# Kernel optimization log

Measured on AMD Instinct MI355X. Metric: run time of the kernel, lower is better.

The kernel has to match this reference:

```python
import jax, jax.numpy as jnp
import numpy as np

H, FFN, NH = 1024, 4096, 16
DK = H // NH
SCALE = DK ** -0.5


def _ln(x, g, b, eps=1e-5):
    m = jnp.mean(x, axis=-1, keepdims=True)
    v = jnp.var(x, axis=-1, keepdims=True)
    return (x - m) * jax.lax.rsqrt(v + eps) * g + b


def setup_inputs() -> dict:
    key = jax.random.key(0)
    ks = jax.random.split(key, 16)
    B, S = 4, 2048
    s = lambda fan: fan ** -0.5
    d = {
        "x": jax.random.normal(ks[0], (B, S, H), jnp.float32),
        "attn_bias": jax.random.normal(ks[1], (1, NH, S, S), jnp.float32),
        "ln1_g": jnp.ones((H,), jnp.float32),
        "ln1_b": jnp.zeros((H,), jnp.float32),
        "Wq": jax.random.normal(ks[2], (H, H), jnp.float32) * s(H),
        "bq": jnp.zeros((H,), jnp.float32),
        "Wk": jax.random.normal(ks[3], (H, H), jnp.float32) * s(H),
        "bk": jnp.zeros((H,), jnp.float32),
        "Wv": jax.random.normal(ks[4], (H, H), jnp.float32) * s(H),
        "bv": jnp.zeros((H,), jnp.float32),
        "Wo": jax.random.normal(ks[5], (H, H), jnp.float32) * s(H),
        "bo": jnp.zeros((H,), jnp.float32),
        "ln2_g": jnp.ones((H,), jnp.float32),
        "ln2_b": jnp.zeros((H,), jnp.float32),
        "W1": jax.random.normal(ks[6], (H, FFN), jnp.float32) * s(H),
        "b1": jnp.zeros((FFN,), jnp.float32),
        "W2": jax.random.normal(ks[7], (FFN, H), jnp.float32) * s(FFN),
        "b2": jnp.zeros((H,), jnp.float32),
    }
    return d


def reference(x, attn_bias, ln1_g, ln1_b, Wq, bq, Wk, bk, Wv, bv, Wo, bo,
              ln2_g, ln2_b, W1, b1, W2, b2):
    B, S, _ = x.shape
    y = _ln(x, ln1_g, ln1_b)
    q = (y @ Wq + bq).reshape(B, S, NH, DK)
    k = (y @ Wk + bk).reshape(B, S, NH, DK)
    v = (y @ Wv + bv).reshape(B, S, NH, DK)
    scores = jnp.einsum("bqhd,bkhd->bhqk", q * SCALE, k) + attn_bias
    A = jax.nn.softmax(scores, axis=-1)
    out = jnp.einsum("bhqk,bkhd->bqhd", A, v).reshape(B, S, H)
    x = x + (out @ Wo + bo)
    y = _ln(x, ln2_g, ln2_b)
    y = jax.nn.gelu(y @ W1 + b1, approximate=False) @ W2 + b2
    return x + y
```

## Files before the change

kernel.cpp:

```cpp
#include <hip/hip_runtime.h>

#define DEVINL __device__ __forceinline__

typedef __bf16 bf16x8 __attribute__((ext_vector_type(8)));
typedef float f32x4 __attribute__((ext_vector_type(4)));
typedef unsigned short u16x4 __attribute__((ext_vector_type(4)));

static constexpr int Bb = 4, S = 2048, H = 1024, NH = 16, DK = 64, FF = 4096;
static constexpr int Mrows = Bb * S;
static constexpr int QS = 3 * H;

DEVINL unsigned short f2bf(float f) {
    union { __bf16 b; unsigned short u; } r;
    r.b = (__bf16)f;
    return r.u;
}

DEVINL unsigned pack_bf2(float a, float b) {
    union { __bf16 h[2]; unsigned u; } r;
    r.h[0] = (__bf16)a; r.h[1] = (__bf16)b;
    return r.u;
}

DEVINL void gld16(const void* g, void* l) {
    auto gp = reinterpret_cast<const __attribute__((address_space(1))) unsigned*>(
        reinterpret_cast<unsigned long long>(g));
    auto lp = reinterpret_cast<__attribute__((address_space(3))) unsigned*>(
        (unsigned)reinterpret_cast<unsigned long long>(l));
    __builtin_amdgcn_global_load_lds(gp, lp, 16, 0, 0);
}

__global__ __launch_bounds__(256)
void wcvt_all(const float* __restrict__ Wq, const float* __restrict__ Wk,
              const float* __restrict__ Wv, const float* __restrict__ Wo,
              const float* __restrict__ W1, const float* __restrict__ W2,
              const float* __restrict__ bq, const float* __restrict__ bk2,
              const float* __restrict__ bv2,
              unsigned short* __restrict__ Wqt, unsigned short* __restrict__ Wot,
              unsigned short* __restrict__ W1t, unsigned short* __restrict__ W2t,
              float* __restrict__ bqkv) {
    int id = blockIdx.x;
    if (id >= 12288) {
        int i = (id - 12288) * 256 + threadIdx.y * 32 + threadIdx.x;
        float v = (i < 1024) ? bq[i] : (i < 2048 ? bk2[i - 1024] : bv2[i - 2048]);
        bqkv[i] = v;
        return;
    }
    const float* in; unsigned short* out; int K, N;
    if (id < 3072) {
        int which = id >> 10; id &= 1023;
        in = which == 0 ? Wq : (which == 1 ? Wk : Wv);
        out = Wqt + (size_t)which * H * H; K = H; N = H;
    } else if (id < 4096) { in = Wo; out = Wot; K = H; N = H; id -= 3072; }
    else if (id < 8192)   { in = W1; out = W1t; K = H; N = FF; id -= 4096; }
    else                  { in = W2; out = W2t; K = FF; N = H; id -= 8192; }
    const int nx = N / 32;
    const int n0 = (id % nx) * 32, k0 = (id / nx) * 32;

    __shared__ float t[32][33];
    int tx = threadIdx.x, ty = threadIdx.y;
#pragma unroll
    for (int i = 0; i < 32; i += 8) t[ty + i][tx] = in[(size_t)(k0 + ty + i) * N + n0 + tx];
    __syncthreads();
#pragma unroll
    for (int i = 0; i < 32; i += 8) out[(size_t)(n0 + ty + i) * K + k0 + tx] = f2bf(t[tx][ty + i]);
}

__global__ __launch_bounds__(256)
void ln_kernel(const float* __restrict__ x, const float* __restrict__ g,
               const float* __restrict__ be, unsigned short* __restrict__ y) {
    int row = blockIdx.x, tid = threadIdx.x;
    const float4 v = ((const float4*)(x + (size_t)row * H))[tid];
    float s = v.x + v.y + v.z + v.w;
    float ss = v.x * v.x + v.y * v.y + v.z * v.z + v.w * v.w;
#pragma unroll
    for (int m = 1; m < 64; m <<= 1) { s += __shfl_xor(s, m); ss += __shfl_xor(ss, m); }
    __shared__ float red[2][4];
    int lane = tid & 63, w = tid >> 6;
    if (lane == 0) { red[0][w] = s; red[1][w] = ss; }
    __syncthreads();
    s = red[0][0] + red[0][1] + red[0][2] + red[0][3];
    ss = red[1][0] + red[1][1] + red[1][2] + red[1][3];
    float mean = s * (1.f / H);
    float var = ss * (1.f / H) - mean * mean;
    float rstd = rsqrtf(var + 1e-5f);
    float4 gv = ((const float4*)g)[tid];
    float4 bv = ((const float4*)be)[tid];
    ushort4 o;
    o.x = f2bf((v.x - mean) * rstd * gv.x + bv.x);
    o.y = f2bf((v.y - mean) * rstd * gv.y + bv.y);
    o.z = f2bf((v.z - mean) * rstd * gv.z + bv.z);
    o.w = f2bf((v.w - mean) * rstd * gv.w + bv.w);
    ((ushort4*)(y + (size_t)row * H))[tid] = o;
}

template <int EPI>
__global__ __launch_bounds__(512, 2)
void gemm8p(const unsigned short* __restrict__ A, const unsigned short* __restrict__ Bt,
            const float* __restrict__ bias, void* __restrict__ outp, int N, int K) {
    __shared__ __align__(16) char lds[131072];
    const int tid = threadIdx.x, lane = tid & 63, w = tid >> 6;
    const int wm = w >> 2, wn = w & 3;
    const int fr = lane & 15, fq = lane >> 4;
    const int nwg = gridDim.x, id = blockIdx.x;
    const int swz = (id & 7) * (nwg >> 3) + (id >> 3);
    const int m0 = (swz & 31) * 256, n0 = (swz >> 5) * 256;

    int srow[2], scol[2];
#pragma unroll
    for (int l = 0; l < 2; ++l) {
        int idx = l * 512 + tid;
        srow[l] = idx >> 3;
        scol[l] = ((idx & 7) ^ (srow[l] & 7)) * 8;
    }
    const int NT = K >> 6;

    auto stage = [&](int ht, int buf, int kt) {
        const unsigned short* src = (ht < 2) ? A : Bt;
        const int hh = ht & 1;
        char* dst = lds + ((ht < 2 ? 0 : 65536) + (buf * 2 + hh) * 16384);
        const int rbase = ((ht < 2) ? m0 : n0) + hh * 128;
        const int kb = kt * 64;
#pragma unroll
        for (int l = 0; l < 2; ++l)
            gld16(src + (size_t)(rbase + srow[l]) * K + kb + scol[l],
                  dst + (size_t)(l * 512 + tid) * 16);
    };

    int oa[2];
#pragma unroll
    for (int ks = 0; ks < 2; ++ks)
        oa[ks] = fr * 128 + (((ks * 4 + fq) ^ (fr & 7)) & 7) * 16;
    const int aBase0 = wm * 16384;
    const int bBase0 = 65536 + (wn >> 1) * 16384 + (wn & 1) * 8192;

    f32x4 acc[8][4] = {};
    bf16x8 aF[4][2], bF[4][2];

    stage(0, 0, 0); stage(1, 0, 0); stage(2, 0, 0); stage(3, 0, 0);
    if (NT > 1) {
        stage(0, 1, 1);
        asm volatile("s_waitcnt vmcnt(2)" ::: "memory");
    } else {
        asm volatile("s_waitcnt vmcnt(0)" ::: "memory");
    }
    __builtin_amdgcn_s_barrier();

    int buf = 0;
    for (int t = 0; t < NT; ++t, buf ^= 1) {
        const char* Ar = lds + aBase0 + buf * 32768;
        const char* Br = lds + bBase0 + buf * 32768;

#pragma unroll
        for (int mb = 0; mb < 4; ++mb)
#pragma unroll
            for (int ks = 0; ks < 2; ++ks)
                aF[mb][ks] = *(const bf16x8*)(Ar + mb * 2048 + oa[ks]);
#pragma unroll
        for (int nb = 0; nb < 2; ++nb)
#pragma unroll
            for (int ks = 0; ks < 2; ++ks)
                bF[nb][ks] = *(const bf16x8*)(Br + nb * 2048 + oa[ks]);
        if (t + 1 < NT) stage(1, buf ^ 1, t + 1);
        __builtin_amdgcn_s_barrier();
        asm volatile("s_waitcnt lgkmcnt(0)" ::: "memory");
        __builtin_amdgcn_sched_barrier(0);
        __builtin_amdgcn_s_setprio(1);
#pragma unroll
        for (int mb = 0; mb < 4; ++mb)
#pragma unroll
            for (int nb = 0; nb < 2; ++nb)
#pragma unroll
                for (int ks = 0; ks < 2; ++ks)
                    acc[mb][nb] = __builtin_amdgcn_mfma_f32_16x16x32_bf16(aF[mb][ks], bF[nb][ks], acc[mb][nb], 0, 0, 0);
        __builtin_amdgcn_s_setprio(0);
        __builtin_amdgcn_s_barrier();

#pragma unroll
        for (int nb = 2; nb < 4; ++nb)
#pragma unroll
            for (int ks = 0; ks < 2; ++ks)
                bF[nb][ks] = *(const bf16x8*)(Br + nb * 2048 + oa[ks]);
        if (t + 1 < NT) stage(2, buf ^ 1, t + 1);
        __builtin_amdgcn_s_barrier();
        asm volatile("s_waitcnt lgkmcnt(0)" ::: "memory");
        __builtin_amdgcn_sched_barrier(0);
        __builtin_amdgcn_s_setprio(1);
#pragma unroll
        for (int mb = 0; mb < 4; ++mb)
#pragma unroll
            for (int nb = 2; nb < 4; ++nb)
#pragma unroll
                for (int ks = 0; ks < 2; ++ks)
                    acc[mb][nb] = __builtin_amdgcn_mfma_f32_16x16x32_bf16(aF[mb][ks], bF[nb][ks], acc[mb][nb], 0, 0, 0);
        __builtin_amdgcn_s_setprio(0);
        __builtin_amdgcn_s_barrier();

#pragma unroll
        for (int mb = 0; mb < 4; ++mb)
#pragma unroll
            for (int ks = 0; ks < 2; ++ks)
                aF[mb][ks] = *(const bf16x8*)(Ar + 8192 + mb * 2048 + oa[ks]);
        if (t + 1 < NT) stage(3, buf ^ 1, t + 1);
        __builtin_amdgcn_s_barrier();
        asm volatile("s_waitcnt lgkmcnt(0)" ::: "memory");
        __builtin_amdgcn_sched_barrier(0);
        __builtin_amdgcn_s_setprio(1);
#pragma unroll
        for (int mb = 0; mb < 4; ++mb)
#pragma unroll
            for (int nb = 0; nb < 2; ++nb)
#pragma unroll
                for (int ks = 0; ks < 2; ++ks)
                    acc[4 + mb][nb] = __builtin_amdgcn_mfma_f32_16x16x32_bf16(aF[mb][ks], bF[nb][ks], acc[4 + mb][nb], 0, 0, 0);
        __builtin_amdgcn_s_setprio(0);
        __builtin_amdgcn_s_barrier();

        if (t + 2 < NT) {
            stage(0, buf, t + 2);
            asm volatile("s_waitcnt vmcnt(2)" ::: "memory");
        } else if (t + 1 < NT) {
            asm volatile("s_waitcnt vmcnt(0)" ::: "memory");
        }
        __builtin_amdgcn_s_barrier();
        __builtin_amdgcn_s_setprio(1);
#pragma unroll
        for (int mb = 0; mb < 4; ++mb)
#pragma unroll
            for (int nb = 2; nb < 4; ++nb)
#pragma unroll
                for (int ks = 0; ks < 2; ++ks)
                    acc[4 + mb][nb] = __builtin_amdgcn_mfma_f32_16x16x32_bf16(aF[mb][ks], bF[nb][ks], acc[4 + mb][nb], 0, 0, 0);
        __builtin_amdgcn_s_setprio(0);
        __builtin_amdgcn_s_barrier();
    }

#pragma unroll
    for (int mb = 0; mb < 8; ++mb) {
        int row0 = m0 + wm * 128 + mb * 16 + fq * 4;
#pragma unroll
        for (int nb = 0; nb < 4; ++nb) {
            int col = n0 + wn * 64 + nb * 16 + fr;
            float bz = bias[col];
#pragma unroll
            for (int j = 0; j < 4; ++j) {
                float vv = acc[mb][nb][j] + bz;
                size_t idx = (size_t)(row0 + j) * N + col;
                if (EPI == 0) {
                    ((unsigned short*)outp)[idx] = f2bf(vv);
                } else {
                    float tg = 0.5f * vv * (1.f + erff(vv * 0.70710678118654752f));
                    ((unsigned short*)outp)[idx] = f2bf(tg);
                }
            }
        }
    }
}

template <int EPI>
__global__ __launch_bounds__(512, 2)
void gemm8p128(const unsigned short* __restrict__ A, const unsigned short* __restrict__ Bt,
               const float* __restrict__ bias, const float* __restrict__ resid,
               void* __restrict__ outp, int N, int K) {
    __shared__ __align__(16) char lds[98304];
    const int tid = threadIdx.x, lane = tid & 63, w = tid >> 6;
    const int wm = w >> 2, wn = w & 3;
    const int fr = lane & 15, fq = lane >> 4;
    const int nwg = gridDim.x, id = blockIdx.x;
    const int swz = (id & 7) * (nwg >> 3) + (id >> 3);
    const int m0 = (swz & 63) * 128, n0 = (swz >> 6) * 256;

    int srow[2], scol[2];
#pragma unroll
    for (int l = 0; l < 2; ++l) {
        int idx = l * 512 + tid;
        srow[l] = idx >> 3;
        scol[l] = ((idx & 7) ^ (srow[l] & 7)) * 8;
    }
    const int NT = K >> 6;

    auto stageA = [&](int buf, int kt) {
        char* dst = lds + buf * 16384;
#pragma unroll
        for (int l = 0; l < 2; ++l)
            gld16(A + (size_t)(m0 + srow[l]) * K + kt * 64 + scol[l],
                  dst + (size_t)(l * 512 + tid) * 16);
    };
    auto stageB = [&](int hh, int buf, int kt) {
        char* dst = lds + 32768 + buf * 32768 + hh * 16384;
#pragma unroll
        for (int l = 0; l < 2; ++l)
            gld16(Bt + (size_t)(n0 + hh * 128 + srow[l]) * K + kt * 64 + scol[l],
                  dst + (size_t)(l * 512 + tid) * 16);
    };

    int oa[2];
#pragma unroll
    for (int ks = 0; ks < 2; ++ks)
        oa[ks] = fr * 128 + (((ks * 4 + fq) ^ (fr & 7)) & 7) * 16;
    const int aWB = wm * 8192;
    const int bWB = (wn >> 1) * 16384 + (wn & 1) * 8192;

    f32x4 acc[4][4] = {};
    bf16x8 aF[2][2], bF[4][2];

    stageA(0, 0); stageB(0, 0, 0); stageB(1, 0, 0);
    if (NT > 1) {
        stageA(1, 1);
        asm volatile("s_waitcnt vmcnt(2)" ::: "memory");
    } else {
        asm volatile("s_waitcnt vmcnt(0)" ::: "memory");
    }
    __builtin_amdgcn_s_barrier();

    int buf = 0;
    for (int t = 0; t < NT; ++t, buf ^= 1) {
        const char* Ar = lds + buf * 16384 + aWB;
        const char* Br = lds + 32768 + buf * 32768 + bWB;

#pragma unroll
        for (int mb = 0; mb < 2; ++mb)
#pragma unroll
            for (int ks = 0; ks < 2; ++ks)
                aF[mb][ks] = *(const bf16x8*)(Ar + mb * 2048 + oa[ks]);
#pragma unroll
        for (int nb = 0; nb < 2; ++nb)
#pragma unroll
            for (int ks = 0; ks < 2; ++ks)
                bF[nb][ks] = *(const bf16x8*)(Br + nb * 2048 + oa[ks]);
        if (t + 1 < NT) stageB(0, buf ^ 1, t + 1);
        __builtin_amdgcn_s_barrier();
        asm volatile("s_waitcnt lgkmcnt(0)" ::: "memory");
        __builtin_amdgcn_sched_barrier(0);
        __builtin_amdgcn_s_setprio(1);
#pragma unroll
        for (int mb = 0; mb < 2; ++mb)
#pragma unroll
            for (int nb = 0; nb < 2; ++nb)
#pragma unroll
                for (int ks = 0; ks < 2; ++ks)
                    acc[mb][nb] = __builtin_amdgcn_mfma_f32_16x16x32_bf16(aF[mb][ks], bF[nb][ks], acc[mb][nb], 0, 0, 0);
        __builtin_amdgcn_s_setprio(0);
        __builtin_amdgcn_s_barrier();

#pragma unroll
        for (int nb = 2; nb < 4; ++nb)
#pragma unroll
            for (int ks = 0; ks < 2; ++ks)
                bF[nb][ks] = *(const bf16x8*)(Br + nb * 2048 + oa[ks]);
        if (t + 1 < NT) stageB(1, buf ^ 1, t + 1);
        __builtin_amdgcn_s_barrier();
        asm volatile("s_waitcnt lgkmcnt(0)" ::: "memory");
        __builtin_amdgcn_sched_barrier(0);
        __builtin_amdgcn_s_setprio(1);
#pragma unroll
        for (int mb = 0; mb < 2; ++mb)
#pragma unroll
            for (int nb = 2; nb < 4; ++nb)
#pragma unroll
                for (int ks = 0; ks < 2; ++ks)
                    acc[mb][nb] = __builtin_amdgcn_mfma_f32_16x16x32_bf16(aF[mb][ks], bF[nb][ks], acc[mb][nb], 0, 0, 0);
        __builtin_amdgcn_s_setprio(0);
        __builtin_amdgcn_s_barrier();

#pragma unroll
        for (int mb = 0; mb < 2; ++mb)
#pragma unroll
            for (int ks = 0; ks < 2; ++ks)
                aF[mb][ks] = *(const bf16x8*)(Ar + 4096 + mb * 2048 + oa[ks]);
        __builtin_amdgcn_s_barrier();
        asm volatile("s_waitcnt lgkmcnt(0)" ::: "memory");
        __builtin_amdgcn_sched_barrier(0);
        __builtin_amdgcn_s_setprio(1);
#pragma unroll
        for (int mb = 0; mb < 2; ++mb)
#pragma unroll
            for (int nb = 0; nb < 2; ++nb)
#pragma unroll
                for (int ks = 0; ks < 2; ++ks)
                    acc[2 + mb][nb] = __builtin_amdgcn_mfma_f32_16x16x32_bf16(aF[mb][ks], bF[nb][ks], acc[2 + mb][nb], 0, 0, 0);
        __builtin_amdgcn_s_setprio(0);
        __builtin_amdgcn_s_barrier();

        if (t + 2 < NT) {
            stageA(buf, t + 2);
            asm volatile("s_waitcnt vmcnt(2)" ::: "memory");
        } else if (t + 1 < NT) {
            asm volatile("s_waitcnt vmcnt(0)" ::: "memory");
        }
        __builtin_amdgcn_s_barrier();
        __builtin_amdgcn_s_setprio(1);
#pragma unroll
        for (int mb = 0; mb < 2; ++mb)
#pragma unroll
            for (int nb = 2; nb < 4; ++nb)
#pragma unroll
                for (int ks = 0; ks < 2; ++ks)
                    acc[2 + mb][nb] = __builtin_amdgcn_mfma_f32_16x16x32_bf16(aF[mb][ks], bF[nb][ks], acc[2 + mb][nb], 0, 0, 0);
        __builtin_amdgcn_s_setprio(0);
        __builtin_amdgcn_s_barrier();
    }

#pragma unroll
    for (int mb = 0; mb < 4; ++mb) {
        int row0 = m0 + wm * 64 + mb * 16 + fq * 4;
#pragma unroll
        for (int nb = 0; nb < 4; ++nb) {
            int col = n0 + wn * 64 + nb * 16 + fr;
            float bz = bias[col];
#pragma unroll
            for (int j = 0; j < 4; ++j) {
                size_t idx = (size_t)(row0 + j) * N + col;
                float vv = acc[mb][nb][j] + bz;
                if (EPI == 0) {
                    ((unsigned short*)outp)[idx] = f2bf(vv);
                } else {
                    ((float*)outp)[idx] = vv + resid[idx];
                }
            }
        }
    }
}

__global__ __launch_bounds__(512, 4)
void attn_kernel(const unsigned short* __restrict__ QKV, const float* __restrict__ bias,
                 unsigned short* __restrict__ O) {
    __shared__ __align__(16) unsigned short lK[3][4096];
    __shared__ __align__(16) unsigned short lV[3][4096];
    const int tid = threadIdx.x, lane = tid & 63, w = tid >> 6;
    const int fr = lane & 15, fq = lane >> 4;

    const int bid = blockIdx.x;
    const int slice = (bid >> 5) * 8 + (bid & 7);
    const int b = (bid >> 3) & 3;
    const int h = slice >> 4;
    const int q0 = (slice & 15) * 128;

    const size_t base = (size_t)b * S * QS + h * DK;
    const unsigned short* Qp = QKV + base;
    const unsigned short* Kp = QKV + base + H;
    const unsigned short* Vp = QKV + base + 2 * H;
    const size_t obase = (size_t)b * S * H + h * DK;

    bf16x8 aq[2];
    {
        const unsigned short* qp = Qp + (size_t)(q0 + w * 16 + fr) * QS + fq * 8;
        aq[0] = *(const bf16x8*)qp;
        aq[1] = *(const bf16x8*)(qp + 32);
    }

    const int chk = w * 64 + lane;
    const int rK = chk >> 3, cK = ((chk & 7) ^ (rK & 7)) * 8;
    int vk, vd;
    {
        int ch = chk;
        int dch = ch & 1, j = (ch >> 1) & 3, fqi = (ch >> 3) & 3, half = (ch >> 5) & 1,
            c = (ch >> 6) & 3, ks = (ch >> 8) & 1;
        vk = ks * 32 + half * 16 + fqi * 4 + j; vd = c * 16 + dch * 8;
    }

    f32x4 oacc[4] = {};
    float lrun = 0.f;
    const float* bias_q = bias + (size_t)h * S * S + (size_t)(q0 + w * 16 + fr) * S;

    const float SC = 0.18033688f;
    const float BL = 1.44269504f;
    const float CC = -23.08312065f;

    auto stage = [&](int buf, int k0) {
        gld16(Kp + (size_t)(k0 + rK) * QS + cK, &lK[buf][w * 512]);
        gld16(Vp + (size_t)(k0 + vk) * QS + vd, &lV[buf][w * 512]);
    };

    union pa_t { unsigned u[4]; bf16x8 v; };
    pa_t pa0, pa1;

    stage(0, 0);
    __syncthreads();
    stage(1, 64);

    {
        float4 bv4[4];
#pragma unroll
        for (int c = 0; c < 4; ++c)
            bv4[c] = *(const float4*)(bias_q + c * 16 + fq * 4);
        f32x4 sacc[4] = {};
        __builtin_amdgcn_s_setprio(1);
#pragma unroll
        for (int c = 0; c < 4; ++c) {
            int row = c * 16 + fr;
#pragma unroll
            for (int dh = 0; dh < 2; ++dh) {
                bf16x8 bk = *(const bf16x8*)((char*)&lK[0][0] +
                    ((row * 128 + dh * 64 + fq * 16) ^ ((row & 7) << 4)));
                sacc[c] = __builtin_amdgcn_mfma_f32_16x16x32_bf16(bk, aq[dh], sacc[c], 0, 0, 0);
            }
        }
        __builtin_amdgcn_s_setprio(0);
        float p[4][4];
#pragma unroll
        for (int c = 0; c < 4; ++c) {
            float b0 = fmaf(bv4[c].x, BL, CC);
            float b1 = fmaf(bv4[c].y, BL, CC);
            float b2 = fmaf(bv4[c].z, BL, CC);
            float b3 = fmaf(bv4[c].w, BL, CC);
            p[c][0] = exp2f(fmaf(sacc[c][0], SC, b0));
            p[c][1] = exp2f(fmaf(sacc[c][1], SC, b1));
            p[c][2] = exp2f(fmaf(sacc[c][2], SC, b2));
            p[c][3] = exp2f(fmaf(sacc[c][3], SC, b3));
            lrun += p[c][0] + p[c][1] + p[c][2] + p[c][3];
        }
        pa0.u[0] = pack_bf2(p[0][0], p[0][1]);
        pa0.u[1] = pack_bf2(p[0][2], p[0][3]);
        pa0.u[2] = pack_bf2(p[1][0], p[1][1]);
        pa0.u[3] = pack_bf2(p[1][2], p[1][3]);
        pa1.u[0] = pack_bf2(p[2][0], p[2][1]);
        pa1.u[1] = pack_bf2(p[2][2], p[2][3]);
        pa1.u[2] = pack_bf2(p[3][0], p[3][1]);
        pa1.u[3] = pack_bf2(p[3][2], p[3][3]);
    }

    int bST = 2, bQK = 1, bPV = 0;
    for (int kt = 1; kt < S / 64; ++kt) {
        __syncthreads();
        if (kt + 1 < S / 64) stage(bST, (kt + 1) * 64);

        float4 bv4[4];
#pragma unroll
        for (int c = 0; c < 4; ++c)
            bv4[c] = *(const float4*)(bias_q + kt * 64 + c * 16 + fq * 4);

        u16x4 ra0[4], rb0[4], ra1[4], rb1[4];
        {
            const char* v0 = (const char*)&lV[bPV][0];
            const char* v1 = v0 + 4096;
#pragma unroll
            for (int c = 0; c < 4; ++c) {
                unsigned ad = (unsigned)(unsigned long long)(v0 + c * 1024) + lane * 8;
                asm volatile("ds_read_b64_tr_b16 %0, %1" : "=&v"(ra0[c]) : "v"(ad));
                asm volatile("ds_read_b64_tr_b16 %0, %1 offset:512" : "=&v"(rb0[c]) : "v"(ad));
            }
#pragma unroll
            for (int c = 0; c < 4; ++c) {
                unsigned ad = (unsigned)(unsigned long long)(v1 + c * 1024) + lane * 8;
                asm volatile("ds_read_b64_tr_b16 %0, %1" : "=&v"(ra1[c]) : "v"(ad));
                asm volatile("ds_read_b64_tr_b16 %0, %1 offset:512" : "=&v"(rb1[c]) : "v"(ad));
            }
        }
        __builtin_amdgcn_sched_barrier(0);

        f32x4 sacc[4] = {};
        __builtin_amdgcn_s_setprio(1);
#pragma unroll
        for (int c = 0; c < 4; ++c) {
            int row = c * 16 + fr;
#pragma unroll
            for (int dh = 0; dh < 2; ++dh) {
                bf16x8 bk = *(const bf16x8*)((char*)&lK[bQK][0] +
                    ((row * 128 + dh * 64 + fq * 16) ^ ((row & 7) << 4)));
                sacc[c] = __builtin_amdgcn_mfma_f32_16x16x32_bf16(bk, aq[dh], sacc[c], 0, 0, 0);
            }
        }
        __builtin_amdgcn_s_setprio(0);

        {
            asm volatile("s_waitcnt lgkmcnt(0)" ::: "memory");
            __builtin_amdgcn_sched_barrier(0);
            __builtin_amdgcn_s_setprio(1);
#pragma unroll
            for (int c = 0; c < 4; ++c) {
                union { u16x4 h2[2]; bf16x8 v8; } u;
                u.h2[0] = ra0[c]; u.h2[1] = rb0[c];
                oacc[c] = __builtin_amdgcn_mfma_f32_16x16x32_bf16(pa0.v, u.v8, oacc[c], 0, 0, 0);
            }
#pragma unroll
            for (int c = 0; c < 4; ++c) {
                union { u16x4 h2[2]; bf16x8 v8; } u;
                u.h2[0] = ra1[c]; u.h2[1] = rb1[c];
                oacc[c] = __builtin_amdgcn_mfma_f32_16x16x32_bf16(pa1.v, u.v8, oacc[c], 0, 0, 0);
            }
            __builtin_amdgcn_s_setprio(0);
            __builtin_amdgcn_sched_barrier(0);
        }

        {
            float p[4][4];
#pragma unroll
            for (int c = 0; c < 4; ++c) {
                float b0 = fmaf(bv4[c].x, BL, CC);
                float b1 = fmaf(bv4[c].y, BL, CC);
                float b2 = fmaf(bv4[c].z, BL, CC);
                float b3 = fmaf(bv4[c].w, BL, CC);
                p[c][0] = exp2f(fmaf(sacc[c][0], SC, b0));
                p[c][1] = exp2f(fmaf(sacc[c][1], SC, b1));
                p[c][2] = exp2f(fmaf(sacc[c][2], SC, b2));
                p[c][3] = exp2f(fmaf(sacc[c][3], SC, b3));
                lrun += p[c][0] + p[c][1] + p[c][2] + p[c][3];
            }
            pa0.u[0] = pack_bf2(p[0][0], p[0][1]);
            pa0.u[1] = pack_bf2(p[0][2], p[0][3]);
            pa0.u[2] = pack_bf2(p[1][0], p[1][1]);
            pa0.u[3] = pack_bf2(p[1][2], p[1][3]);
            pa1.u[0] = pack_bf2(p[2][0], p[2][1]);
            pa1.u[1] = pack_bf2(p[2][2], p[2][3]);
            pa1.u[2] = pack_bf2(p[3][0], p[3][1]);
            pa1.u[3] = pack_bf2(p[3][2], p[3][3]);
        }

        bPV = bQK; bQK = bST; bST = (bST == 2) ? 0 : bST + 1;
    }

    {
        const char* v0 = (const char*)&lV[bPV][0];
        const char* v1 = v0 + 4096;
        u16x4 ra0[4], rb0[4], ra1[4], rb1[4];
#pragma unroll
        for (int c = 0; c < 4; ++c) {
            unsigned ad = (unsigned)(unsigned long long)(v0 + c * 1024) + lane * 8;
            asm volatile("ds_read_b64_tr_b16 %0, %1" : "=&v"(ra0[c]) : "v"(ad));
            asm volatile("ds_read_b64_tr_b16 %0, %1 offset:512" : "=&v"(rb0[c]) : "v"(ad));
        }
#pragma unroll
        for (int c = 0; c < 4; ++c) {
            unsigned ad = (unsigned)(unsigned long long)(v1 + c * 1024) + lane * 8;
            asm volatile("ds_read_b64_tr_b16 %0, %1" : "=&v"(ra1[c]) : "v"(ad));
            asm volatile("ds_read_b64_tr_b16 %0, %1 offset:512" : "=&v"(rb1[c]) : "v"(ad));
        }
        asm volatile("s_waitcnt lgkmcnt(0)" ::: "memory");
        __builtin_amdgcn_sched_barrier(0);
        __builtin_amdgcn_s_setprio(1);
#pragma unroll
        for (int c = 0; c < 4; ++c) {
            union { u16x4 h2[2]; bf16x8 v8; } u;
            u.h2[0] = ra0[c]; u.h2[1] = rb0[c];
            oacc[c] = __builtin_amdgcn_mfma_f32_16x16x32_bf16(pa0.v, u.v8, oacc[c], 0, 0, 0);
        }
#pragma unroll
        for (int c = 0; c < 4; ++c) {
            union { u16x4 h2[2]; bf16x8 v8; } u;
            u.h2[0] = ra1[c]; u.h2[1] = rb1[c];
            oacc[c] = __builtin_amdgcn_mfma_f32_16x16x32_bf16(pa1.v, u.v8, oacc[c], 0, 0, 0);
        }
        __builtin_amdgcn_s_setprio(0);
    }

    lrun += __shfl_xor(lrun, 16);
    lrun += __shfl_xor(lrun, 32);
    float linv = 1.f / lrun;
    float lo[4];
#pragma unroll
    for (int j = 0; j < 4; ++j) lo[j] = __shfl(linv, fq * 4 + j);
#pragma unroll
    for (int c = 0; c < 4; ++c)
#pragma unroll
        for (int j = 0; j < 4; ++j) {
            int row = q0 + w * 16 + fq * 4 + j;
            int d = c * 16 + fr;
            O[obase + (size_t)row * H + d] = f2bf(oacc[c][j] * lo[j]);
        }
}

extern "C" void kernel_launch(void* const* d_in, const int* in_sizes, int n_in,
                              void* d_out, int out_size, void* d_ws, size_t ws_size,
                              hipStream_t stream) {
    const float* x    = (const float*)d_in[0];
    const float* ab   = (const float*)d_in[1];
    const float* ln1g = (const float*)d_in[2];
    const float* ln1b = (const float*)d_in[3];
    const float* Wq   = (const float*)d_in[4];
    const float* bq   = (const float*)d_in[5];
    const float* Wk   = (const float*)d_in[6];
    const float* bk   = (const float*)d_in[7];
    const float* Wv   = (const float*)d_in[8];
    const float* bv   = (const float*)d_in[9];
    const float* Wo   = (const float*)d_in[10];
    const float* bo   = (const float*)d_in[11];
    const float* ln2g = (const float*)d_in[12];
    const float* ln2b = (const float*)d_in[13];
    const float* W1   = (const float*)d_in[14];
    const float* b1   = (const float*)d_in[15];
    const float* W2   = (const float*)d_in[16];
    const float* b2   = (const float*)d_in[17];

    char* ws = (char*)d_ws;
    size_t off = 0;
    auto alloc = [&](size_t bytes) -> void* {
        void* p = ws + off;
        off += (bytes + 255) & ~(size_t)255;
        return p;
    };
    unsigned short* Wqt = (unsigned short*)alloc((size_t)H * H * 2);
    unsigned short* Wkt = (unsigned short*)alloc((size_t)H * H * 2);
    unsigned short* Wvt = (unsigned short*)alloc((size_t)H * H * 2);
    unsigned short* Wot = (unsigned short*)alloc((size_t)H * H * 2);
    unsigned short* W1t = (unsigned short*)alloc((size_t)H * FF * 2);
    unsigned short* W2t = (unsigned short*)alloc((size_t)H * FF * 2);
    float* bqkv        = (float*)alloc((size_t)QS * 4);
    unsigned short* ybuf = (unsigned short*)alloc((size_t)Mrows * H * 2);
    unsigned short* qkvb = (unsigned short*)alloc((size_t)Mrows * QS * 2);
    unsigned short* ob = (unsigned short*)alloc((size_t)Mrows * H * 2);
    unsigned short* hb = (unsigned short*)alloc((size_t)Mrows * FF * 2);
    (void)ws_size; (void)in_sizes; (void)n_in; (void)out_size;
    (void)Wkt; (void)Wvt;

    dim3 tb(32, 8, 1);
    wcvt_all<<<dim3(12300), tb, 0, stream>>>(Wq, Wk, Wv, Wo, W1, W2, bq, bk, bv,
                                             Wqt, Wot, W1t, W2t, bqkv);

    ln_kernel<<<Mrows, 256, 0, stream>>>(x, ln1g, ln1b, ybuf);

    gemm8p128<0><<<dim3((Mrows / 128) * (QS / 256)), 512, 0, stream>>>(ybuf, Wqt, bqkv, nullptr, qkvb, QS, H);

    attn_kernel<<<dim3(Bb * NH * (S / 128)), 512, 0, stream>>>(qkvb, ab, ob);

    gemm8p128<2><<<dim3((Mrows / 128) * (H / 256)), 512, 0, stream>>>(ob, Wot, bo, x, d_out, H, H);

    ln_kernel<<<Mrows, 256, 0, stream>>>((const float*)d_out, ln2g, ln2b, ybuf);

    gemm8p<1><<<dim3((Mrows / 256) * (FF / 256)), 512, 0, stream>>>(ybuf, W1t, b1, hb, FF, H);

    gemm8p128<2><<<dim3((Mrows / 128) * (H / 256)), 512, 0, stream>>>(hb, W2t, b2, (const float*)d_out, d_out, H, FF);
}
```

Measured before the change: 512.0 us.

## Process two KV tiles per barrier with five-buffer LDS ring in attention

The attention loop now handles two 64-key tiles per __syncthreads, using a 5-deep shared-memory ring for K and V and staging two tiles ahead per outer iteration. The goal is to halve the number of block-wide barriers and deepen global-load prefetch. In exchange, LDS use grows from 48KB to 80KB per block, which may reduce how many blocks fit on each CU (launch bounds ask for 4).

```diff
diff --git a/kernel.cpp b/kernel.cpp
--- a/kernel.cpp
+++ b/kernel.cpp
@@ -425,8 +425,8 @@
 __global__ __launch_bounds__(512, 4)
 void attn_kernel(const unsigned short* __restrict__ QKV, const float* __restrict__ bias,
                  unsigned short* __restrict__ O) {
-    __shared__ __align__(16) unsigned short lK[3][4096];
-    __shared__ __align__(16) unsigned short lV[3][4096];
+    __shared__ __align__(16) unsigned short lK[5][4096];
+    __shared__ __align__(16) unsigned short lV[5][4096];
     const int tid = threadIdx.x, lane = tid & 63, w = tid >> 6;
     const int fr = lane & 15, fq = lane >> 4;
 
@@ -475,15 +475,31 @@
     union pa_t { unsigned u[4]; bf16x8 v; };
     pa_t pa0, pa1;
 
-    stage(0, 0);
-    __syncthreads();
-    stage(1, 64);
-
-    {
+    auto SUB = [&](int kt, int kb, int vb) {
         float4 bv4[4];
 #pragma unroll
         for (int c = 0; c < 4; ++c)
-            bv4[c] = *(const float4*)(bias_q + c * 16 + fq * 4);
+            bv4[c] = *(const float4*)(bias_q + kt * 64 + c * 16 + fq * 4);
+
+        u16x4 ra0[4], rb0[4], ra1[4], rb1[4];
+        {
+            const char* v0 = (const char*)&lV[vb][0];
+            const char* v1 = v0 + 4096;
+#pragma unroll
+            for (int c = 0; c < 4; ++c) {
+                unsigned ad = (unsigned)(unsigned long long)(v0 + c * 1024) + lane * 8;
+                asm volatile("ds_read_b64_tr_b16 %0, %1" : "=&v"(ra0[c]) : "v"(ad));
+                asm volatile("ds_read_b64_tr_b16 %0, %1 offset:512" : "=&v"(rb0[c]) : "v"(ad));
+            }
+#pragma unroll
+            for (int c = 0; c < 4; ++c) {
+                unsigned ad = (unsigned)(unsigned long long)(v1 + c * 1024) + lane * 8;
+                asm volatile("ds_read_b64_tr_b16 %0, %1" : "=&v"(ra1[c]) : "v"(ad));
+                asm volatile("ds_read_b64_tr_b16 %0, %1 offset:512" : "=&v"(rb1[c]) : "v"(ad));
+            }
+        }
+        __builtin_amdgcn_sched_barrier(0);
+
         f32x4 sacc[4] = {};
         __builtin_amdgcn_s_setprio(1);
 #pragma unroll
@@ -491,12 +507,31 @@
             int row = c * 16 + fr;
 #pragma unroll
             for (int dh = 0; dh < 2; ++dh) {
-                bf16x8 bk = *(const bf16x8*)((char*)&lK[0][0] +
+                bf16x8 bk = *(const bf16x8*)((char*)&lK[kb][0] +
                     ((row * 128 + dh * 64 + fq * 16) ^ ((row & 7) << 4)));
                 sacc[c] = __builtin_amdgcn_mfma_f32_16x16x32_bf16(bk, aq[dh], sacc[c], 0, 0, 0);
             }
         }
         __builtin_amdgcn_s_setprio(0);
+
+        asm volatile("s_waitcnt lgkmcnt(0)" ::: "memory");
+        __builtin_amdgcn_sched_barrier(0);
+        __builtin_amdgcn_s_setprio(1);
+#pragma unroll
+        for (int c = 0; c < 4; ++c) {
+            union { u16x4 h2[2]; bf16x8 v8; } u;
+            u.h2[0] = ra0[c]; u.h2[1] = rb0[c];
+            oacc[c] = __builtin_amdgcn_mfma_f32_16x16x32_bf16(pa0.v, u.v8, oacc[c], 0, 0, 0);
+        }
+#pragma unroll
+        for (int c = 0; c < 4; ++c) {
+            union { u16x4 h2[2]; bf16x8 v8; } u;
+            u.h2[0] = ra1[c]; u.h2[1] = rb1[c];
+            oacc[c] = __builtin_amdgcn_mfma_f32_16x16x32_bf16(pa1.v, u.v8, oacc[c], 0, 0, 0);
+        }
+        __builtin_amdgcn_s_setprio(0);
+        __builtin_amdgcn_sched_barrier(0);
+
         float p[4][4];
 #pragma unroll
         for (int c = 0; c < 4; ++c) {
@@ -518,37 +553,17 @@
         pa1.u[1] = pack_bf2(p[2][2], p[2][3]);
         pa1.u[2] = pack_bf2(p[3][0], p[3][1]);
         pa1.u[3] = pack_bf2(p[3][2], p[3][3]);
-    }
-
-    int bST = 2, bQK = 1, bPV = 0;
-    for (int kt = 1; kt < S / 64; ++kt) {
-        __syncthreads();
-        if (kt + 1 < S / 64) stage(bST, (kt + 1) * 64);
-
+    };
+
+    stage(0, 0);
+    stage(1, 64);
+    __syncthreads();
+    stage(2, 128);
+    {
         float4 bv4[4];
 #pragma unroll
         for (int c = 0; c < 4; ++c)
-            bv4[c] = *(const float4*)(bias_q + kt * 64 + c * 16 + fq * 4);
-
-        u16x4 ra0[4], rb0[4], ra1[4], rb1[4];
-        {
-            const char* v0 = (const char*)&lV[bPV][0];
-            const char* v1 = v0 + 4096;
-#pragma unroll
-            for (int c = 0; c < 4; ++c) {
-                unsigned ad = (unsigned)(unsigned long long)(v0 + c * 1024) + lane * 8;
-                asm volatile("ds_read_b64_tr_b16 %0, %1" : "=&v"(ra0[c]) : "v"(ad));
-                asm volatile("ds_read_b64_tr_b16 %0, %1 offset:512" : "=&v"(rb0[c]) : "v"(ad));
-            }
-#pragma unroll
-            for (int c = 0; c < 4; ++c) {
-                unsigned ad = (unsigned)(unsigned long long)(v1 + c * 1024) + lane * 8;
-                asm volatile("ds_read_b64_tr_b16 %0, %1" : "=&v"(ra1[c]) : "v"(ad));
-                asm volatile("ds_read_b64_tr_b16 %0, %1 offset:512" : "=&v"(rb1[c]) : "v"(ad));
-            }
-        }
-        __builtin_amdgcn_sched_barrier(0);
-
+            bv4[c] = *(const float4*)(bias_q + c * 16 + fq * 4);
         f32x4 sacc[4] = {};
         __builtin_amdgcn_s_setprio(1);
 #pragma unroll
@@ -556,62 +571,55 @@
             int row = c * 16 + fr;
 #pragma unroll
             for (int dh = 0; dh < 2; ++dh) {
-                bf16x8 bk = *(const bf16x8*)((char*)&lK[bQK][0] +
+                bf16x8 bk = *(const bf16x8*)((char*)&lK[0][0] +
                     ((row * 128 + dh * 64 + fq * 16) ^ ((row & 7) << 4)));
                 sacc[c] = __builtin_amdgcn_mfma_f32_16x16x32_bf16(bk, aq[dh], sacc[c], 0, 0, 0);
             }
         }
         __builtin_amdgcn_s_setprio(0);
-
-        {
-            asm volatile("s_waitcnt lgkmcnt(0)" ::: "memory");
-            __builtin_amdgcn_sched_barrier(0);
-            __builtin_amdgcn_s_setprio(1);
-#pragma unroll
-            for (int c = 0; c < 4; ++c) {
-                union { u16x4 h2[2]; bf16x8 v8; } u;
-                u.h2[0] = ra0[c]; u.h2[1] = rb0[c];
-                oacc[c] = __builtin_amdgcn_mfma_f32_16x16x32_bf16(pa0.v, u.v8, oacc[c], 0, 0, 0);
-            }
-#pragma unroll
-            for (int c = 0; c < 4; ++c) {
-                union { u16x4 h2[2]; bf16x8 v8; } u;
-                u.h2[0] = ra1[c]; u.h2[1] = rb1[c];
-                oacc[c] = __builtin_amdgcn_mfma_f32_16x16x32_bf16(pa1.v, u.v8, oacc[c], 0, 0, 0);
-            }
-            __builtin_amdgcn_s_setprio(0);
-            __builtin_amdgcn_sched_barrier(0);
-        }
-
-        {
-            float p[4][4];
-#pragma unroll
-            for (int c = 0; c < 4; ++c) {
-                float b0 = fmaf(bv4[c].x, BL, CC);
-                float b1 = fmaf(bv4[c].y, BL, CC);
-                float b2 = fmaf(bv4[c].z, BL, CC);
-                float b3 = fmaf(bv4[c].w, BL, CC);
-                p[c][0] = exp2f(fmaf(sacc[c][0], SC, b0));
-                p[c][1] = exp2f(fmaf(sacc[c][1], SC, b1));
-                p[c][2] = exp2f(fmaf(sacc[c][2], SC, b2));
-                p[c][3] = exp2f(fmaf(sacc[c][3], SC, b3));
-                lrun += p[c][0] + p[c][1] + p[c][2] + p[c][3];
-            }
-            pa0.u[0] = pack_bf2(p[0][0], p[0][1]);
-            pa0.u[1] = pack_bf2(p[0][2], p[0][3]);
-            pa0.u[2] = pack_bf2(p[1][0], p[1][1]);
-            pa0.u[3] = pack_bf2(p[1][2], p[1][3]);
-            pa1.u[0] = pack_bf2(p[2][0], p[2][1]);
-            pa1.u[1] = pack_bf2(p[2][2], p[2][3]);
-            pa1.u[2] = pack_bf2(p[3][0], p[3][1]);
-            pa1.u[3] = pack_bf2(p[3][2], p[3][3]);
-        }
-
-        bPV = bQK; bQK = bST; bST = (bST == 2) ? 0 : bST + 1;
-    }
-
+        float p[4][4];
+#pragma unroll
+        for (int c = 0; c < 4; ++c) {
+            float b0 = fmaf(bv4[c].x, BL, CC);
+            float b1 = fmaf(bv4[c].y, BL, CC);
+            float b2 = fmaf(bv4[c].z, BL, CC);
+            float b3 = fmaf(bv4[c].w, BL, CC);
+            p[c][0] = exp2f(fmaf(sacc[c][0], SC, b0));
+            p[c][1] = exp2f(fmaf(sacc[c][1], SC, b1));
+            p[c][2] = exp2f(fmaf(sacc[c][2], SC, b2));
+            p[c][3] = exp2f(fmaf(sacc[c][3], SC, b3));
+            lrun += p[c][0] + p[c][1] + p[c][2] + p[c][3];
+        }
+        pa0.u[0] = pack_bf2(p[0][0], p[0][1]);
+        pa0.u[1] = pack_bf2(p[0][2], p[0][3]);
+        pa0.u[2] = pack_bf2(p[1][0], p[1][1]);
+        pa0.u[3] = pack_bf2(p[1][2], p[1][3]);
+        pa1.u[0] = pack_bf2(p[2][0], p[2][1]);
+        pa1.u[1] = pack_bf2(p[2][2], p[2][3]);
+        pa1.u[2] = pack_bf2(p[3][0], p[3][1]);
+        pa1.u[3] = pack_bf2(p[3][2], p[3][3]);
+    }
+
+    int m0b = 0;
+    for (int i = 0; i < 15; ++i) {
+        const int t2 = 2 * i;
+        const int m1 = (m0b + 1 < 5) ? m0b + 1 : m0b - 4;
+        const int m2 = (m1 + 1 < 5) ? m1 + 1 : m1 - 4;
+        const int m3 = (m2 + 1 < 5) ? m2 + 1 : m2 - 4;
+        const int m4 = (m3 + 1 < 5) ? m3 + 1 : m3 - 4;
+        __syncthreads();
+        stage(m3, (t2 + 3) * 64);
+        if (t2 + 4 < 32) stage(m4, (t2 + 4) * 64);
+        SUB(t2 + 1, m1, m0b);
+        SUB(t2 + 2, m2, m1);
+        m0b = m2;
+    }
+
+    __syncthreads();
     {
-        const char* v0 = (const char*)&lV[bPV][0];
+        const int m1 = (m0b + 1 < 5) ? m0b + 1 : m0b - 4;
+        SUB(31, m1, m0b);
+        const char* v0 = (const char*)&lV[m1][0];
         const char* v1 = v0 + 4096;
         u16x4 ra0[4], rb0[4], ra1[4], rb1[4];
 #pragma unroll
```

Result: slower. 544.2 us (+6.3%).
